# Kernel optimization log

Hardware: AMD Instinct MI355X
Metric: run time of the kernel (lower is better)

## Reference

```python
import jax, jax.numpy as jnp
import numpy as np

N_EMBED = 512  # scaling uses n_embed**-0.5 (as in the original, not head_dim)

def setup_inputs() -> dict:
    key = jax.random.key(0)
    k1, k2, k3 = jax.random.split(key, 3)
    B, T, HD = 4, 4096, 64
    return {
        "k": jax.random.normal(k1, (B, T, HD), dtype=jnp.float32),
        "q": jax.random.normal(k2, (B, T, HD), dtype=jnp.float32),
        "v": jax.random.normal(k3, (B, T, HD), dtype=jnp.float32),
    }

def reference(k, q, v):
    # wei = q @ k^T * n_embed^-0.5  -> [B, T, T]
    scale = N_EMBED ** (-0.5)
    wei = jnp.einsum("bqd,bkd->bqk", q, k) * scale
    T = q.shape[1]
    causal = jnp.tril(jnp.ones((T, T), dtype=bool))  # [T, T]
    wei = jnp.where(causal, wei, -jnp.inf)
    wei = jax.nn.softmax(wei, axis=-1)
    # dropout p=0.0 (identity)
    out = jnp.einsum("bqk,bkd->bqd", wei, v)
    return out
```

## Files before the change

kernel.cpp:

```cpp
#include <hip/hip_runtime.h>
#include <hip/hip_bf16.h>
#include <math.h>


typedef __attribute__((ext_vector_type(8))) __bf16 bf16x8;
typedef __attribute__((ext_vector_type(8))) short  short8;
typedef __attribute__((ext_vector_type(4))) float  f32x4;

#define TT 4096
#define DD 64
#define CH 6
#define NCHUNK_PB 374
#define NSLOT (NCHUNK_PB * 4)

static constexpr float SCALE_L2E = 0.06375871665087779f;

__device__ __forceinline__ ushort f2bf(float x) {
    return __builtin_bit_cast(ushort, (__bf16)x);
}

__global__ __launch_bounds__(256, 1)
void prep(const float* __restrict__ K, const float* __restrict__ V,
          ushort* __restrict__ Kbf, ushort* __restrict__ Vtbf) {
    const int bx = blockIdx.x;
    const int b = bx & 3, kt = bx >> 2;
    const size_t tbase = (size_t)bx * 4096;
    const size_t gbase = (size_t)b * TT * DD + (size_t)(kt << 6) * DD;
    const int tid = threadIdx.x;

    {
        const int row = tid >> 2, q4 = tid & 3;
        const float* src = K + gbase + row * 64 + q4 * 16;
        ushort* dst = Kbf + tbase + row * 64;
        #pragma unroll
        for (int h = 0; h < 2; ++h) {
            f32x4 x = *(const f32x4*)(src + h * 8);
            f32x4 y = *(const f32x4*)(src + h * 8 + 4);
            union { ushort u[8]; short8 s; } pk;
            #pragma unroll
            for (int j = 0; j < 4; ++j) {
                pk.u[j]     = f2bf(x[j]);
                pk.u[j + 4] = f2bf(y[j]);
            }
            const int ch = (q4 * 2 + h) ^ (row & 7);
            *(short8*)(dst + ch * 8) = pk.s;
        }
    }
    {
        const int kp = tid & 31, dg = tid >> 5;
        const float* v0 = V + gbase + dg * 8 + kp * 2 * 64;
        f32x4 a0 = *(const f32x4*)(v0);
        f32x4 a1 = *(const f32x4*)(v0 + 4);
        f32x4 b0 = *(const f32x4*)(v0 + 64);
        f32x4 b1 = *(const f32x4*)(v0 + 68);
        #pragma unroll
        for (int j = 0; j < 8; ++j) {
            float xa = (j < 4) ? a0[j & 3] : a1[j & 3];
            float xb = (j < 4) ? b0[j & 3] : b1[j & 3];
            unsigned pk2 = (unsigned)f2bf(xa) | ((unsigned)f2bf(xb) << 16);
            const int dim = dg * 8 + j;
            const int off = dim * 64 + (((kp >> 2) ^ j) << 3) + ((kp * 2) & 7);
            *(unsigned*)(Vtbf + tbase + off) = pk2;
        }
    }
}

__global__ __launch_bounds__(256, 1)
void attn_part(const ushort* __restrict__ Kbf, const float* __restrict__ Q,
               const ushort* __restrict__ Vtbf,
               float* __restrict__ Opart, float* __restrict__ Lpart) {
    const int bx = blockIdx.x;
    const int b  = bx & 3;
    const int chunkid = bx >> 2;
    int o = 0, base = 0;
    for (;;) {
        const int cnt = ((o == 10) ? 4 : 6) * (o + 1);
        if (chunkid < base + cnt) break;
        base += cnt; ++o;
    }
    const int within = chunkid - base;
    const int qi = within / (o + 1);
    const int qt = o * 6 + qi;
    const int chunk = within - qi * (o + 1);

    const int qbase = qt << 6;
    const int tid = threadIdx.x;
    const int w = tid >> 6, lane = tid & 63;
    const int g = lane >> 4, c = lane & 15;
    const int qr0 = qbase + (w << 4);

    __shared__ ushort lKV[2][2][4096];
    __shared__ ushort lP [4][16 * 64];

    const int kt0 = chunk * CH;
    const int kt1 = min(kt0 + CH, qt + 1);

    const int seg0 = w * 1024;
    const int loff = lane * 8;

    {
        const size_t tb = (size_t)((kt0 << 2) | b) * 4096;
        #pragma unroll
        for (int p = 0; p < 2; ++p) {
            const int seg = seg0 + p * 512;
            __builtin_amdgcn_global_load_lds(
                (const __attribute__((address_space(1))) void*)(Kbf + tb + seg + loff),
                (__attribute__((address_space(3))) void*)&lKV[0][0][seg], 16, 0, 0);
            __builtin_amdgcn_global_load_lds(
                (const __attribute__((address_space(1))) void*)(Vtbf + tb + seg + loff),
                (__attribute__((address_space(3))) void*)&lKV[0][1][seg], 16, 0, 0);
        }
    }

    bf16x8 qf[2];
    {
        const float* qp = Q + (size_t)b * TT * DD + (size_t)(qr0 + c) * DD + g * 8;
        #pragma unroll
        for (int ks = 0; ks < 2; ++ks) {
            f32x4 a = *(const f32x4*)(qp + ks * 32);
            f32x4 d = *(const f32x4*)(qp + ks * 32 + 4);
            bf16x8 t;
            #pragma unroll
            for (int j = 0; j < 4; ++j) {
                t[j]     = (__bf16)(a[j] * SCALE_L2E);
                t[j + 4] = (__bf16)(d[j] * SCALE_L2E);
            }
            qf[ks] = t;
        }
    }

    f32x4 acc[4];
    #pragma unroll
    for (int nt = 0; nt < 4; ++nt) acc[nt] = (f32x4){0.f, 0.f, 0.f, 0.f};
    float l_r[4] = {0.f, 0.f, 0.f, 0.f};

    for (int kt = kt0; kt < kt1; ++kt) {
        const int kb = kt << 6;
        const int cur = (kt - kt0) & 1;

        __syncthreads();

        if (kt + 1 < kt1) {
            const size_t tb = (size_t)(((kt + 1) << 2) | b) * 4096;
            #pragma unroll
            for (int p = 0; p < 2; ++p) {
                const int seg = seg0 + p * 512;
                __builtin_amdgcn_global_load_lds(
                    (const __attribute__((address_space(1))) void*)(Kbf + tb + seg + loff),
                    (__attribute__((address_space(3))) void*)&lKV[cur ^ 1][0][seg], 16, 0, 0);
                __builtin_amdgcn_global_load_lds(
                    (const __attribute__((address_space(1))) void*)(Vtbf + tb + seg + loff),
                    (__attribute__((address_space(3))) void*)&lKV[cur ^ 1][1][seg], 16, 0, 0);
            }
        }

        if (kb <= qr0 + 15) {
            const ushort* lK  = lKV[cur][0];
            const ushort* lVt = lKV[cur][1];
            f32x4 S[4];
            #pragma unroll
            for (int nt = 0; nt < 4; ++nt) {
                const int row = nt * 16 + c;
                bf16x8 kf0 = __builtin_bit_cast(bf16x8,
                    *(const short8*)&lK[row * 64 + (((0 * 4 + g) ^ (c & 7)) << 3)]);
                bf16x8 kf1 = __builtin_bit_cast(bf16x8,
                    *(const short8*)&lK[row * 64 + (((1 * 4 + g) ^ (c & 7)) << 3)]);
                f32x4 s = (f32x4){0.f, 0.f, 0.f, 0.f};
                s = __builtin_amdgcn_mfma_f32_16x16x32_bf16(qf[0], kf0, s, 0, 0, 0);
                s = __builtin_amdgcn_mfma_f32_16x16x32_bf16(qf[1], kf1, s, 0, 0, 0);
                S[nt] = s;
            }
            if (kb + 63 > qr0) {
                #pragma unroll
                for (int nt = 0; nt < 4; ++nt)
                    #pragma unroll
                    for (int r = 0; r < 4; ++r)
                        if (kb + nt * 16 + c > qr0 + g * 4 + r) S[nt][r] = -INFINITY;
            }
            f32x4 P[4];
            #pragma unroll
            for (int nt = 0; nt < 4; ++nt)
                #pragma unroll
                for (int r = 0; r < 4; ++r)
                    P[nt][r] = exp2f(S[nt][r]);
            float ps[4];
            #pragma unroll
            for (int r = 0; r < 4; ++r)
                ps[r] = (P[0][r] + P[1][r]) + (P[2][r] + P[3][r]);
            #pragma unroll
            for (int off = 8; off >= 1; off >>= 1)
                #pragma unroll
                for (int r = 0; r < 4; ++r)
                    ps[r] += __shfl_xor(ps[r], off);
            #pragma unroll
            for (int r = 0; r < 4; ++r)
                l_r[r] += ps[r];
            ushort* myP = lP[w];
            #pragma unroll
            for (int nt = 0; nt < 4; ++nt)
                #pragma unroll
                for (int r = 0; r < 4; ++r) {
                    const int row = g * 4 + r;
                    const int col = nt * 16 + c;
                    myP[row * 64 + (((col >> 3) ^ (row & 7)) << 3) + (col & 7)] =
                        f2bf(P[nt][r]);
                }
            #pragma unroll
            for (int ks = 0; ks < 2; ++ks) {
                bf16x8 pf = __builtin_bit_cast(bf16x8,
                    *(const short8*)&myP[c * 64 + (((ks * 4 + g) ^ (c & 7)) << 3)]);
                #pragma unroll
                for (int nt = 0; nt < 4; ++nt) {
                    bf16x8 vf = __builtin_bit_cast(bf16x8,
                        *(const short8*)&lVt[(nt * 16 + c) * 64 + (((ks * 4 + g) ^ (c & 7)) << 3)]);
                    acc[nt] = __builtin_amdgcn_mfma_f32_16x16x32_bf16(pf, vf, acc[nt], 0, 0, 0);
                }
            }
        }
    }

    const int slot = bx;
    #pragma unroll
    for (int r = 0; r < 4; ++r) {
        const int row = (w << 4) + g * 4 + r;
        #pragma unroll
        for (int nt = 0; nt < 4; ++nt)
            Opart[(size_t)slot * 4096 + row * 64 + nt * 16 + c] = acc[nt][r];
        if (c == 0)
            Lpart[slot * 64 + row] = l_r[r];
    }
}

__global__ __launch_bounds__(256, 1)
void attn_merge(const float* __restrict__ Opart, const float* __restrict__ Lpart,
                float* __restrict__ Out) {
    const int bx = blockIdx.x;
    const int b = bx & 3, qt = (bx >> 2) & 63, qq = bx >> 8;
    const int o = qt / 6, nch = o + 1;
    const int cbase = 3 * o * (o + 1) + (qt - 6 * o) * nch;
    const int tid = threadIdx.x;
    const int r = tid >> 2, d0 = qq * 16 + (tid & 3) * 4;

    f32x4 ov = (f32x4){0.f, 0.f, 0.f, 0.f};
    float lt = 0.f;
    for (int cix = 0; cix < nch; ++cix) {
        const int slot = (cbase + cix) * 4 + b;
        lt += Lpart[(size_t)slot * 64 + r];
        f32x4 x = *(const f32x4*)(Opart + (size_t)slot * 4096 + r * 64 + d0);
        #pragma unroll
        for (int e = 0; e < 4; ++e) ov[e] += x[e];
    }
    const float inv = 1.0f / lt;
    f32x4 res;
    #pragma unroll
    for (int e = 0; e < 4; ++e) res[e] = ov[e] * inv;
    *(f32x4*)(Out + (size_t)b * TT * DD + (size_t)((qt << 6) + r) * DD + d0) = res;
}

__global__ __launch_bounds__(256, 1)
void attn_head(const float* __restrict__ K, const float* __restrict__ Q,
               const float* __restrict__ V, float* __restrict__ Out) {
    const int bx = blockIdx.x;
    const int b  = bx & 3;
    const int qt = bx >> 2;
    const int qbase = qt << 6;
    const int tid = threadIdx.x;
    const int w = tid >> 6, lane = tid & 63;
    const int g = lane >> 4, c = lane & 15;
    const int qr0 = qbase + (w << 4);

    __shared__ ushort lK [64 * 64];
    __shared__ ushort lVt[64 * 64];
    __shared__ ushort lP [4][16 * 64];

    const size_t bbase = (size_t)b * TT * DD;
    bf16x8 qf[2];
    {
        const float* qp = Q + bbase + (size_t)(qr0 + c) * DD + g * 8;
        #pragma unroll
        for (int ks = 0; ks < 2; ++ks) {
            f32x4 a = *(const f32x4*)(qp + ks * 32);
            f32x4 d = *(const f32x4*)(qp + ks * 32 + 4);
            bf16x8 t;
            #pragma unroll
            for (int j = 0; j < 4; ++j) {
                t[j]     = (__bf16)(a[j] * SCALE_L2E);
                t[j + 4] = (__bf16)(d[j] * SCALE_L2E);
            }
            qf[ks] = t;
        }
    }
    f32x4 acc[4];
    #pragma unroll
    for (int nt = 0; nt < 4; ++nt) acc[nt] = (f32x4){0.f, 0.f, 0.f, 0.f};
    float l_r[4] = {0.f, 0.f, 0.f, 0.f};
    const int e0  = w * 1024 + lane * 8;
    const int kch = ((lane & 7) ^ ((lane >> 3) & 7)) << 3;
    const int kp  = tid & 31, dg = tid >> 5;
    const int nkt = qt + 1;
    for (int kt = 0; kt < nkt; ++kt) {
        const int kb = kt << 6;
        __syncthreads();
        {
            const float* src = K + bbase + (size_t)kb * DD;
            #pragma unroll
            for (int p = 0; p < 2; ++p) {
                const int e = e0 + p * 512;
                f32x4 x = *(const f32x4*)(src + e);
                f32x4 y = *(const f32x4*)(src + e + 4);
                union { ushort u[8]; short8 s; } pk;
                #pragma unroll
                for (int j = 0; j < 4; ++j) {
                    pk.u[j]     = f2bf(x[j]);
                    pk.u[j + 4] = f2bf(y[j]);
                }
                *(short8*)&lK[(e >> 6) * 64 + kch] = pk.s;
            }
        }
        {
            const float* v0 = V + bbase + (size_t)kb * DD + dg * 8 + kp * 2 * 64;
            f32x4 a0 = *(const f32x4*)(v0);
            f32x4 a1 = *(const f32x4*)(v0 + 4);
            f32x4 b0 = *(const f32x4*)(v0 + 64);
            f32x4 b1 = *(const f32x4*)(v0 + 68);
            #pragma unroll
            for (int j = 0; j < 8; ++j) {
                float xa = (j < 4) ? a0[j & 3] : a1[j & 3];
                float xb = (j < 4) ? b0[j & 3] : b1[j & 3];
                unsigned pk2 = (unsigned)f2bf(xa) | ((unsigned)f2bf(xb) << 16);
                const int dim = dg * 8 + j;
                const int off = dim * 64 + (((kp >> 2) ^ j) << 3) + ((kp * 2) & 7);
                *(unsigned*)&lVt[off] = pk2;
            }
        }
        __syncthreads();
        if (kb <= qr0 + 15) {
            f32x4 S[4];
            #pragma unroll
            for (int nt = 0; nt < 4; ++nt) {
                const int row = nt * 16 + c;
                bf16x8 kf0 = __builtin_bit_cast(bf16x8,
                    *(const short8*)&lK[row * 64 + (((0 * 4 + g) ^ (c & 7)) << 3)]);
                bf16x8 kf1 = __builtin_bit_cast(bf16x8,
                    *(const short8*)&lK[row * 64 + (((1 * 4 + g) ^ (c & 7)) << 3)]);
                f32x4 s = (f32x4){0.f, 0.f, 0.f, 0.f};
                s = __builtin_amdgcn_mfma_f32_16x16x32_bf16(qf[0], kf0, s, 0, 0, 0);
                s = __builtin_amdgcn_mfma_f32_16x16x32_bf16(qf[1], kf1, s, 0, 0, 0);
                S[nt] = s;
            }
            if (kb + 63 > qr0) {
                #pragma unroll
                for (int nt = 0; nt < 4; ++nt)
                    #pragma unroll
                    for (int r = 0; r < 4; ++r)
                        if (kb + nt * 16 + c > qr0 + g * 4 + r) S[nt][r] = -INFINITY;
            }
            f32x4 P[4];
            #pragma unroll
            for (int nt = 0; nt < 4; ++nt)
                #pragma unroll
                for (int r = 0; r < 4; ++r)
                    P[nt][r] = exp2f(S[nt][r]);
            float ps[4];
            #pragma unroll
            for (int r = 0; r < 4; ++r)
                ps[r] = (P[0][r] + P[1][r]) + (P[2][r] + P[3][r]);
            #pragma unroll
            for (int off = 8; off >= 1; off >>= 1)
                #pragma unroll
                for (int r = 0; r < 4; ++r)
                    ps[r] += __shfl_xor(ps[r], off);
            #pragma unroll
            for (int r = 0; r < 4; ++r)
                l_r[r] += ps[r];
            ushort* myP = lP[w];
            #pragma unroll
            for (int nt = 0; nt < 4; ++nt)
                #pragma unroll
                for (int r = 0; r < 4; ++r) {
                    const int row = g * 4 + r;
                    const int col = nt * 16 + c;
                    myP[row * 64 + (((col >> 3) ^ (row & 7)) << 3) + (col & 7)] =
                        f2bf(P[nt][r]);
                }
            #pragma unroll
            for (int ks = 0; ks < 2; ++ks) {
                bf16x8 pf = __builtin_bit_cast(bf16x8,
                    *(const short8*)&myP[c * 64 + (((ks * 4 + g) ^ (c & 7)) << 3)]);
                #pragma unroll
                for (int nt = 0; nt < 4; ++nt) {
                    bf16x8 vf = __builtin_bit_cast(bf16x8,
                        *(const short8*)&lVt[(nt * 16 + c) * 64 + (((ks * 4 + g) ^ (c & 7)) << 3)]);
                    acc[nt] = __builtin_amdgcn_mfma_f32_16x16x32_bf16(pf, vf, acc[nt], 0, 0, 0);
                }
            }
        }
    }
    #pragma unroll
    for (int r = 0; r < 4; ++r) {
        const float inv = 1.0f / l_r[r];
        const size_t rowoff = bbase + (size_t)(qr0 + g * 4 + r) * DD;
        #pragma unroll
        for (int nt = 0; nt < 4; ++nt)
            Out[rowoff + nt * 16 + c] = acc[nt][r] * inv;
    }
}

extern "C" void kernel_launch(void* const* d_in, const int* in_sizes, int n_in,
                              void* d_out, int out_size, void* d_ws, size_t ws_size,
                              hipStream_t stream) {
    const float* k = (const float*)d_in[0];
    const float* q = (const float*)d_in[1];
    const float* v = (const float*)d_in[2];
    float* out = (float*)d_out;

    const size_t kv_elems = (size_t)4 * 64 * 4096;
    const size_t op_elems = (size_t)NSLOT * 4096;
    const size_t need = kv_elems * 2 * 2 + op_elems * 4 + (size_t)NSLOT * 64 * 4;
    if (ws_size >= need) {
        ushort* Kbf  = (ushort*)d_ws;
        ushort* Vtbf = Kbf + kv_elems;
        float* Opart = (float*)(Vtbf + kv_elems);
        float* Lpart = Opart + op_elems;
        hipLaunchKernelGGL(prep, dim3(256), dim3(256), 0, stream, k, v, Kbf, Vtbf);
        hipLaunchKernelGGL(attn_part, dim3(NSLOT), dim3(256), 0, stream,
                           Kbf, q, Vtbf, Opart, Lpart);
        hipLaunchKernelGGL(attn_merge, dim3(1024), dim3(256), 0, stream,
                           Opart, Lpart, out);
    } else {
        hipLaunchKernelGGL(attn_head, dim3(256), dim3(256), 0, stream, k, q, v, out);
    }
}
```

Baseline: 105.3 us.

## Repartition attention into 128-row query strips with fixed two-tile key chunks

Each attention work item now covers a 128-row query strip against a fixed two-tile (128-key) chunk, giving a triangular enumeration of 528 chunks per batch. Each wave handles 32 query rows and reuses each K/V fragment across two MFMA row blocks. Partial outputs are stored as bf16 and the row-sum shuffle reduction moves to the end, and the merge kernel is rewritten for the new layout. Launch bounds allow 4 blocks per CU for higher occupancy. The cost is more partial slots for the merge to read and extra rounding error from the bf16 partials.

```diff
diff --git a/kernel.cpp b/kernel.cpp
--- a/kernel.cpp
+++ b/kernel.cpp
@@ -9,14 +9,17 @@
 
 #define TT 4096
 #define DD 64
-#define CH 6
-#define NCHUNK_PB 374
+#define NST 32
+#define NCHUNK_PB 528
 #define NSLOT (NCHUNK_PB * 4)
 
 static constexpr float SCALE_L2E = 0.06375871665087779f;
 
 __device__ __forceinline__ ushort f2bf(float x) {
     return __builtin_bit_cast(ushort, (__bf16)x);
+}
+__device__ __forceinline__ float bf2f(ushort u) {
+    return __builtin_bit_cast(float, ((unsigned)u) << 16);
 }
 
 __global__ __launch_bounds__(256, 1)
@@ -65,36 +68,27 @@
     }
 }
 
-__global__ __launch_bounds__(256, 1)
+__global__ __launch_bounds__(256, 4)
 void attn_part(const ushort* __restrict__ Kbf, const float* __restrict__ Q,
                const ushort* __restrict__ Vtbf,
-               float* __restrict__ Opart, float* __restrict__ Lpart) {
+               ushort* __restrict__ Opart, float* __restrict__ Lpart) {
     const int bx = blockIdx.x;
     const int b  = bx & 3;
     const int chunkid = bx >> 2;
-    int o = 0, base = 0;
-    for (;;) {
-        const int cnt = ((o == 10) ? 4 : 6) * (o + 1);
-        if (chunkid < base + cnt) break;
-        base += cnt; ++o;
-    }
-    const int within = chunkid - base;
-    const int qi = within / (o + 1);
-    const int qt = o * 6 + qi;
-    const int chunk = within - qi * (o + 1);
-
-    const int qbase = qt << 6;
+    int s = 0;
+    while (chunkid >= ((s + 1) * (s + 2)) >> 1) ++s;
+    const int chunk = chunkid - ((s * (s + 1)) >> 1);
+
+    const int qs0 = s << 7;
     const int tid = threadIdx.x;
     const int w = tid >> 6, lane = tid & 63;
     const int g = lane >> 4, c = lane & 15;
-    const int qr0 = qbase + (w << 4);
+    const int qw0 = qs0 + (w << 5);
 
     __shared__ ushort lKV[2][2][4096];
-    __shared__ ushort lP [4][16 * 64];
-
-    const int kt0 = chunk * CH;
-    const int kt1 = min(kt0 + CH, qt + 1);
-
+    __shared__ ushort lP [4][1024];
+
+    const int kt0 = chunk * 2;
     const int seg0 = w * 1024;
     const int loff = lane * 8;
 
@@ -112,9 +106,11 @@
         }
     }
 
-    bf16x8 qf[2];
-    {
-        const float* qp = Q + (size_t)b * TT * DD + (size_t)(qr0 + c) * DD + g * 8;
+    bf16x8 qf[2][2];
+    #pragma unroll
+    for (int m = 0; m < 2; ++m) {
+        const float* qp = Q + (size_t)b * TT * DD
+                        + (size_t)(qw0 + m * 16 + c) * DD + g * 8;
         #pragma unroll
         for (int ks = 0; ks < 2; ++ks) {
             f32x4 a = *(const f32x4*)(qp + ks * 32);
@@ -125,136 +121,174 @@
                 t[j]     = (__bf16)(a[j] * SCALE_L2E);
                 t[j + 4] = (__bf16)(d[j] * SCALE_L2E);
             }
-            qf[ks] = t;
-        }
-    }
-
-    f32x4 acc[4];
-    #pragma unroll
-    for (int nt = 0; nt < 4; ++nt) acc[nt] = (f32x4){0.f, 0.f, 0.f, 0.f};
-    float l_r[4] = {0.f, 0.f, 0.f, 0.f};
-
-    for (int kt = kt0; kt < kt1; ++kt) {
+            qf[m][ks] = t;
+        }
+    }
+
+    f32x4 acc[2][4];
+    #pragma unroll
+    for (int m = 0; m < 2; ++m)
+        #pragma unroll
+        for (int nt = 0; nt < 4; ++nt) acc[m][nt] = (f32x4){0.f, 0.f, 0.f, 0.f};
+    float l_p[2][4] = {{0.f,0.f,0.f,0.f},{0.f,0.f,0.f,0.f}};
+
+    #pragma unroll
+    for (int st = 0; st < 2; ++st) {
+        const int kt = kt0 + st;
         const int kb = kt << 6;
-        const int cur = (kt - kt0) & 1;
 
         __syncthreads();
 
-        if (kt + 1 < kt1) {
+        if (st == 0) {
             const size_t tb = (size_t)(((kt + 1) << 2) | b) * 4096;
             #pragma unroll
             for (int p = 0; p < 2; ++p) {
                 const int seg = seg0 + p * 512;
                 __builtin_amdgcn_global_load_lds(
                     (const __attribute__((address_space(1))) void*)(Kbf + tb + seg + loff),
-                    (__attribute__((address_space(3))) void*)&lKV[cur ^ 1][0][seg], 16, 0, 0);
+                    (__attribute__((address_space(3))) void*)&lKV[1][0][seg], 16, 0, 0);
                 __builtin_amdgcn_global_load_lds(
                     (const __attribute__((address_space(1))) void*)(Vtbf + tb + seg + loff),
-                    (__attribute__((address_space(3))) void*)&lKV[cur ^ 1][1][seg], 16, 0, 0);
-            }
-        }
-
-        if (kb <= qr0 + 15) {
-            const ushort* lK  = lKV[cur][0];
-            const ushort* lVt = lKV[cur][1];
-            f32x4 S[4];
-            #pragma unroll
-            for (int nt = 0; nt < 4; ++nt) {
-                const int row = nt * 16 + c;
-                bf16x8 kf0 = __builtin_bit_cast(bf16x8,
-                    *(const short8*)&lK[row * 64 + (((0 * 4 + g) ^ (c & 7)) << 3)]);
-                bf16x8 kf1 = __builtin_bit_cast(bf16x8,
-                    *(const short8*)&lK[row * 64 + (((1 * 4 + g) ^ (c & 7)) << 3)]);
-                f32x4 s = (f32x4){0.f, 0.f, 0.f, 0.f};
-                s = __builtin_amdgcn_mfma_f32_16x16x32_bf16(qf[0], kf0, s, 0, 0, 0);
-                s = __builtin_amdgcn_mfma_f32_16x16x32_bf16(qf[1], kf1, s, 0, 0, 0);
-                S[nt] = s;
-            }
-            if (kb + 63 > qr0) {
+                    (__attribute__((address_space(3))) void*)&lKV[1][1][seg], 16, 0, 0);
+            }
+        }
+
+        if (kb > qw0 + 31) continue;
+        const bool act0 = (kb <= qw0 + 15);
+
+        const ushort* lK  = lKV[st][0];
+        const ushort* lVt = lKV[st][1];
+
+        f32x4 S[2][4];
+        #pragma unroll
+        for (int nt = 0; nt < 4; ++nt) {
+            const int row = nt * 16 + c;
+            bf16x8 kf0 = __builtin_bit_cast(bf16x8,
+                *(const short8*)&lK[row * 64 + (((0 * 4 + g) ^ (c & 7)) << 3)]);
+            bf16x8 kf1 = __builtin_bit_cast(bf16x8,
+                *(const short8*)&lK[row * 64 + (((1 * 4 + g) ^ (c & 7)) << 3)]);
+            #pragma unroll
+            for (int m = 0; m < 2; ++m) {
+                if (m == 0 && !act0) continue;
+                f32x4 sm = (f32x4){0.f, 0.f, 0.f, 0.f};
+                sm = __builtin_amdgcn_mfma_f32_16x16x32_bf16(qf[m][0], kf0, sm, 0, 0, 0);
+                sm = __builtin_amdgcn_mfma_f32_16x16x32_bf16(qf[m][1], kf1, sm, 0, 0, 0);
+                S[m][nt] = sm;
+            }
+        }
+
+        bf16x8 pf[2][2];
+        #pragma unroll
+        for (int m = 0; m < 2; ++m) {
+            if (m == 0 && !act0) continue;
+            const int qm0 = qw0 + m * 16;
+            if (kb + 63 > qm0) {
                 #pragma unroll
                 for (int nt = 0; nt < 4; ++nt)
                     #pragma unroll
                     for (int r = 0; r < 4; ++r)
-                        if (kb + nt * 16 + c > qr0 + g * 4 + r) S[nt][r] = -INFINITY;
-            }
-            f32x4 P[4];
+                        if (kb + nt * 16 + c > qm0 + g * 4 + r) S[m][nt][r] = -INFINITY;
+            }
+            ushort* myP = lP[w];
             #pragma unroll
             for (int nt = 0; nt < 4; ++nt)
                 #pragma unroll
-                for (int r = 0; r < 4; ++r)
-                    P[nt][r] = exp2f(S[nt][r]);
-            float ps[4];
-            #pragma unroll
-            for (int r = 0; r < 4; ++r)
-                ps[r] = (P[0][r] + P[1][r]) + (P[2][r] + P[3][r]);
-            #pragma unroll
-            for (int off = 8; off >= 1; off >>= 1)
-                #pragma unroll
-                for (int r = 0; r < 4; ++r)
-                    ps[r] += __shfl_xor(ps[r], off);
-            #pragma unroll
-            for (int r = 0; r < 4; ++r)
-                l_r[r] += ps[r];
-            ushort* myP = lP[w];
-            #pragma unroll
-            for (int nt = 0; nt < 4; ++nt)
-                #pragma unroll
                 for (int r = 0; r < 4; ++r) {
+                    const float P = exp2f(S[m][nt][r]);
+                    l_p[m][r] += P;
                     const int row = g * 4 + r;
                     const int col = nt * 16 + c;
                     myP[row * 64 + (((col >> 3) ^ (row & 7)) << 3) + (col & 7)] =
-                        f2bf(P[nt][r]);
+                        f2bf(P);
                 }
             #pragma unroll
-            for (int ks = 0; ks < 2; ++ks) {
-                bf16x8 pf = __builtin_bit_cast(bf16x8,
+            for (int ks = 0; ks < 2; ++ks)
+                pf[m][ks] = __builtin_bit_cast(bf16x8,
                     *(const short8*)&myP[c * 64 + (((ks * 4 + g) ^ (c & 7)) << 3)]);
-                #pragma unroll
-                for (int nt = 0; nt < 4; ++nt) {
-                    bf16x8 vf = __builtin_bit_cast(bf16x8,
-                        *(const short8*)&lVt[(nt * 16 + c) * 64 + (((ks * 4 + g) ^ (c & 7)) << 3)]);
-                    acc[nt] = __builtin_amdgcn_mfma_f32_16x16x32_bf16(pf, vf, acc[nt], 0, 0, 0);
+        }
+
+        #pragma unroll
+        for (int ks = 0; ks < 2; ++ks)
+            #pragma unroll
+            for (int nt = 0; nt < 4; ++nt) {
+                bf16x8 vf = __builtin_bit_cast(bf16x8,
+                    *(const short8*)&lVt[(nt * 16 + c) * 64 + (((ks * 4 + g) ^ (c & 7)) << 3)]);
+                #pragma unroll
+                for (int m = 0; m < 2; ++m) {
+                    if (m == 0 && !act0) continue;
+                    acc[m][nt] = __builtin_amdgcn_mfma_f32_16x16x32_bf16(
+                        pf[m][ks], vf, acc[m][nt], 0, 0, 0);
                 }
             }
-        }
     }
 
     const int slot = bx;
     #pragma unroll
-    for (int r = 0; r < 4; ++r) {
-        const int row = (w << 4) + g * 4 + r;
+    for (int m = 0; m < 2; ++m) {
+        #pragma unroll
+        for (int r = 0; r < 4; ++r) {
+            float l = l_p[m][r];
+            #pragma unroll
+            for (int off = 8; off >= 1; off >>= 1)
+                l += __shfl_xor(l, off);
+            l_p[m][r] = l;
+        }
+        union { ushort u[16]; short8 s[2]; } pk;
         #pragma unroll
         for (int nt = 0; nt < 4; ++nt)
-            Opart[(size_t)slot * 4096 + row * 64 + nt * 16 + c] = acc[nt][r];
-        if (c == 0)
-            Lpart[slot * 64 + row] = l_r[r];
+            #pragma unroll
+            for (int r = 0; r < 4; ++r)
+                pk.u[nt * 4 + r] = f2bf(acc[m][nt][r]);
+        ushort* op = Opart + (size_t)slot * 8192 + (w * 2 + m) * 1024 + lane * 16;
+        *(short8*)op       = pk.s[0];
+        *(short8*)(op + 8) = pk.s[1];
+        if (c == 0) {
+            #pragma unroll
+            for (int r = 0; r < 4; ++r)
+                Lpart[(size_t)slot * 128 + w * 32 + m * 16 + g * 4 + r] = l_p[m][r];
+        }
     }
 }
 
 __global__ __launch_bounds__(256, 1)
-void attn_merge(const float* __restrict__ Opart, const float* __restrict__ Lpart,
+void attn_merge(const ushort* __restrict__ Opart, const float* __restrict__ Lpart,
                 float* __restrict__ Out) {
     const int bx = blockIdx.x;
-    const int b = bx & 3, qt = (bx >> 2) & 63, qq = bx >> 8;
-    const int o = qt / 6, nch = o + 1;
-    const int cbase = 3 * o * (o + 1) + (qt - 6 * o) * nch;
+    const int b = bx & 3, s = (bx >> 2) & 31, w = bx >> 7;
     const int tid = threadIdx.x;
-    const int r = tid >> 2, d0 = qq * 16 + (tid & 3) * 4;
-
-    f32x4 ov = (f32x4){0.f, 0.f, 0.f, 0.f};
-    float lt = 0.f;
-    for (int cix = 0; cix < nch; ++cix) {
-        const int slot = (cbase + cix) * 4 + b;
-        lt += Lpart[(size_t)slot * 64 + r];
-        f32x4 x = *(const f32x4*)(Opart + (size_t)slot * 4096 + r * 64 + d0);
-        #pragma unroll
-        for (int e = 0; e < 4; ++e) ov[e] += x[e];
-    }
-    const float inv = 1.0f / lt;
-    f32x4 res;
-    #pragma unroll
-    for (int e = 0; e < 4; ++e) res[e] = ov[e] * inv;
-    *(f32x4*)(Out + (size_t)b * TT * DD + (size_t)((qt << 6) + r) * DD + d0) = res;
+    const int m = tid >> 7, half = (tid >> 6) & 1, lane = tid & 63;
+    const int g = lane >> 4, c = lane & 15;
+    const int cbase = (s * (s + 1)) >> 1;
+    const int nch = s + 1;
+
+    float v[8];
+    #pragma unroll
+    for (int i = 0; i < 8; ++i) v[i] = 0.f;
+    f32x4 lsum = (f32x4){0.f, 0.f, 0.f, 0.f};
+
+    for (int ci = 0; ci < nch; ++ci) {
+        const int slot = (cbase + ci) * 4 + b;
+        const ushort* op = Opart + (size_t)slot * 8192
+                         + (w * 2 + m) * 1024 + lane * 16 + half * 8;
+        short8 sv = *(const short8*)op;
+        #pragma unroll
+        for (int i = 0; i < 8; ++i) v[i] += bf2f((ushort)sv[i]);
+        f32x4 lv = *(const f32x4*)(Lpart + (size_t)slot * 128 + w * 32 + m * 16 + g * 4);
+        #pragma unroll
+        for (int r = 0; r < 4; ++r) lsum[r] += lv[r];
+    }
+
+    f32x4 inv;
+    #pragma unroll
+    for (int r = 0; r < 4; ++r) inv[r] = 1.0f / lsum[r];
+
+    const int qbase = s * 128 + w * 32 + m * 16 + g * 4;
+    float* dst = Out + (size_t)b * TT * DD;
+    #pragma unroll
+    for (int i = 0; i < 8; ++i) {
+        const int nt = half * 2 + (i >> 2), r = i & 3;
+        dst[(size_t)(qbase + r) * DD + nt * 16 + c] = v[i] * inv[r];
+    }
 }
 
 __global__ __launch_bounds__(256, 1)
@@ -343,10 +377,10 @@
                     *(const short8*)&lK[row * 64 + (((0 * 4 + g) ^ (c & 7)) << 3)]);
                 bf16x8 kf1 = __builtin_bit_cast(bf16x8,
                     *(const short8*)&lK[row * 64 + (((1 * 4 + g) ^ (c & 7)) << 3)]);
-                f32x4 s = (f32x4){0.f, 0.f, 0.f, 0.f};
-                s = __builtin_amdgcn_mfma_f32_16x16x32_bf16(qf[0], kf0, s, 0, 0, 0);
-                s = __builtin_amdgcn_mfma_f32_16x16x32_bf16(qf[1], kf1, s, 0, 0, 0);
-                S[nt] = s;
+                f32x4 sv = (f32x4){0.f, 0.f, 0.f, 0.f};
+                sv = __builtin_amdgcn_mfma_f32_16x16x32_bf16(qf[0], kf0, sv, 0, 0, 0);
+                sv = __builtin_amdgcn_mfma_f32_16x16x32_bf16(qf[1], kf1, sv, 0, 0, 0);
+                S[nt] = sv;
             }
             if (kb + 63 > qr0) {
                 #pragma unroll
@@ -415,17 +449,17 @@
     float* out = (float*)d_out;
 
     const size_t kv_elems = (size_t)4 * 64 * 4096;
-    const size_t op_elems = (size_t)NSLOT * 4096;
-    const size_t need = kv_elems * 2 * 2 + op_elems * 4 + (size_t)NSLOT * 64 * 4;
+    const size_t op_elems = (size_t)NSLOT * 8192;
+    const size_t need = kv_elems * 2 * 2 + op_elems * 2 + (size_t)NSLOT * 128 * 4;
     if (ws_size >= need) {
         ushort* Kbf  = (ushort*)d_ws;
         ushort* Vtbf = Kbf + kv_elems;
-        float* Opart = (float*)(Vtbf + kv_elems);
-        float* Lpart = Opart + op_elems;
+        ushort* Opart = Vtbf + kv_elems;
+        float* Lpart = (float*)(Opart + op_elems);
         hipLaunchKernelGGL(prep, dim3(256), dim3(256), 0, stream, k, v, Kbf, Vtbf);
         hipLaunchKernelGGL(attn_part, dim3(NSLOT), dim3(256), 0, stream,
                            Kbf, q, Vtbf, Opart, Lpart);
-        hipLaunchKernelGGL(attn_merge, dim3(1024), dim3(256), 0, stream,
+        hipLaunchKernelGGL(attn_merge, dim3(512), dim3(256), 0, stream,
                            Opart, Lpart, out);
     } else {
         hipLaunchKernelGGL(attn_head, dim3(256), dim3(256), 0, stream, k, q, v, out);
```

Result: no change. 106.3 us (+1.0%).
